# Kernel tuning notes

Measured on AMD Instinct MI355X. Metric: run time of the kernel, lower is better.

## Reference

```python
import jax, jax.numpy as jnp
import numpy as np

N_NODES = 50000
N_EDGES = 640000
HID = 128
EDGE_FEAT = 4
NUM_G = 20
R_MIN, R_MAX = 0.0, 10.0

def setup_inputs() -> dict:
    key = jax.random.key(0)
    ks = jax.random.split(key, 16)
    s = lambda d: 1.0 / np.sqrt(d)
    return {
        'h': jax.random.normal(ks[0], (N_NODES, HID), jnp.float32),
        'x': jax.random.normal(ks[1], (N_NODES, 3), jnp.float32),
        'edge_index': jax.random.randint(ks[2], (2, N_EDGES), 0, N_NODES, dtype=jnp.int64),
        'mask_ligand': jnp.ones((N_NODES,), jnp.float32),
        'edge_attr': jax.random.normal(ks[3], (N_EDGES, EDGE_FEAT), jnp.float32),
        'We1': jax.random.normal(ks[4], (2*HID+EDGE_FEAT+NUM_G, HID), jnp.float32) * s(2*HID+EDGE_FEAT+NUM_G),
        'be1': jnp.zeros((HID,), jnp.float32),
        'We2': jax.random.normal(ks[5], (HID, HID), jnp.float32) * s(HID),
        'be2': jnp.zeros((HID,), jnp.float32),
        'Winf': jax.random.normal(ks[6], (HID, 1), jnp.float32) * s(HID),
        'binf': jnp.zeros((1,), jnp.float32),
        'Wx1': jax.random.normal(ks[7], (HID, HID), jnp.float32) * s(HID),
        'bx1': jnp.zeros((HID,), jnp.float32),
        'Wx2': jax.random.normal(ks[8], (HID, 1), jnp.float32) * 0.001 * s(HID),
        'Wn1': jax.random.normal(ks[9], (2*HID, HID), jnp.float32) * s(2*HID),
        'bn1': jnp.zeros((HID,), jnp.float32),
        'Wn2': jax.random.normal(ks[10], (HID, HID), jnp.float32) * s(HID),
        'bn2': jnp.zeros((HID,), jnp.float32),
    }

def reference(h, x, edge_index, mask_ligand, edge_attr,
              We1, be1, We2, be2, Winf, binf, Wx1, bx1, Wx2, Wn1, bn1, Wn2, bn2):
    n = h.shape[0]
    src, dst = edge_index[0], edge_index[1]
    hi, hj = h[dst], h[src]                      # [E, H] gathers
    rel_x = x[dst] - x[src]                      # [E, 3]
    d_sq = jnp.sum(rel_x**2, axis=-1, keepdims=True)  # [E, 1]
    d = jnp.sqrt(d_sq + 1e-8)
    # GaussianSmearing(r_min=0, r_max=10, num_gaussians=20)
    offset = jnp.linspace(R_MIN, R_MAX, NUM_G, dtype=h.dtype)
    coeff = -0.5 / (offset[1] - offset[0])**2
    d_feat = jnp.exp(coeff * (d - offset)**2)    # [E, 20]
    edge_feat = jnp.concatenate([d_feat, edge_attr], axis=-1)
    # edge MLP (2 layers, silu, act_last=True)
    z = jnp.concatenate([hi, hj, edge_feat], axis=-1)
    mij = jax.nn.silu(jax.nn.silu(z @ We1 + be1) @ We2 + be2)  # [E, H]
    eij = jax.nn.sigmoid(mij @ Winf + binf)      # [E, 1]
    mi = jax.ops.segment_sum(mij * eij, dst, num_segments=n)   # [N, H]
    # node MLP (2 layers, silu, no act on last)
    nz = jnp.concatenate([mi, h], axis=-1)
    h_out = h + (jax.nn.silu(nz @ Wn1 + bn1) @ Wn2 + bn2)
    # coordinate update
    xg = jnp.tanh(jax.nn.silu(mij @ Wx1 + bx1) @ Wx2)          # [E, 1]
    delta_x = jax.ops.segment_sum(rel_x / (d + 1.0) * xg, dst, num_segments=n)
    x_out = x + delta_x * mask_ligand[:, None]
    return h_out, x_out
```

## Files before the change

### kernel.cpp

```cpp
#include <hip/hip_runtime.h>
#include <math.h>

#define NN 50000
#define NE 640000
#define H 128
#define EPB 64
#define NPB 64
#define ZB 296
#define BB 136
#define KP1 288
#define NZB 264
#define NBPAD 50176
#define HISTB (NE / 256)
#define CONVB 464
#define ALLOCB (NBPAD / 256)
#define HCONVB 3125
#define N4OUT ((NN * H + NN * 3) / 4)
#define ZOB ((N4OUT + 255) / 256)

typedef __attribute__((ext_vector_type(8))) unsigned short u16x8;
typedef __attribute__((ext_vector_type(8))) __bf16 bf16x8;
typedef __attribute__((ext_vector_type(2))) __bf16 bf16x2;
typedef __attribute__((ext_vector_type(4))) float f32x4;

__device__ __forceinline__ float frcp(float x) {
#if __has_builtin(__builtin_amdgcn_rcpf)
    return __builtin_amdgcn_rcpf(x);
#else
    return 1.0f / x;
#endif
}

__device__ __forceinline__ float silu_f(float v) {
    return v * frcp(1.0f + __expf(-v));
}

__device__ __forceinline__ float sigmoid_f(float v) {
    return frcp(1.0f + __expf(-v));
}

__device__ __forceinline__ float tanh_f(float v) {
    return 1.0f - 2.0f * frcp(1.0f + __expf(2.0f * v));
}

__device__ __forceinline__ unsigned short f2bf(float f) {
    unsigned int u = __builtin_bit_cast(unsigned int, f);
    u += 0x7FFFu + ((u >> 16) & 1u);
    return (unsigned short)(u >> 16);
}

__device__ __forceinline__ float bf2f(unsigned short s) {
    unsigned int u = ((unsigned int)s) << 16;
    return __builtin_bit_cast(float, u);
}

__device__ __forceinline__ unsigned int pkbf(float lo, float hi) {
#if __has_builtin(__builtin_amdgcn_cvt_pk_bf16_f32)
    bf16x2 v = __builtin_amdgcn_cvt_pk_bf16_f32(lo, hi);
    unsigned int r; __builtin_memcpy(&r, &v, 4); return r;
#else
    return (unsigned int)f2bf(lo) | ((unsigned int)f2bf(hi) << 16);
#endif
}

__device__ __forceinline__ f32x4 mfma16(u16x8 a, u16x8 b, f32x4 c) {
    return __builtin_amdgcn_mfma_f32_16x16x32_bf16(
        __builtin_bit_cast(bf16x8, a), __builtin_bit_cast(bf16x8, b), c, 0, 0, 0);
}

__global__ __launch_bounds__(256) void init_small_kernel(
    float4* __restrict__ p, int n4)
{
    int i = blockIdx.x * 256 + threadIdx.x;
    if (i < n4) p[i] = make_float4(0.f, 0.f, 0.f, 0.f);
}

__global__ __launch_bounds__(256) void hist_conv_zero_hconv_kernel(
    const int* __restrict__ ei, int* __restrict__ cnt, int histBlocks,
    const float* __restrict__ We1, const float* __restrict__ We2,
    const float* __restrict__ Wx1, const float* __restrict__ Wn1,
    const float* __restrict__ Wn2,
    unsigned short* __restrict__ w1t, unsigned short* __restrict__ w2t,
    unsigned short* __restrict__ wx1t, unsigned short* __restrict__ wn1t,
    unsigned short* __restrict__ wn2t,
    float4* __restrict__ out4,
    const float* __restrict__ h, unsigned short* __restrict__ hb)
{
    int b = blockIdx.x, t = threadIdx.x;
    if (b < histBlocks) {
        atomicAdd(&cnt[ei[NE + b * 256 + t]], 1);
        return;
    }
    b -= histBlocks;
    if (b < CONVB) {
        int i = b * 256 + t;
        const int S1 = 128 * KP1;
        const int S2 = 128 * 128;
        const int S3 = 128 * 256;
        if (i < S1) {
            int n = i / KP1, k = i % KP1;
            w1t[i] = (k < 280) ? f2bf(We1[k * H + n]) : (unsigned short)0;
        } else if (i < S1 + S2) {
            int j = i - S1; int n = j / H, k = j % H;
            w2t[j] = f2bf(We2[k * H + n]);
        } else if (i < S1 + 2 * S2) {
            int j = i - S1 - S2; int n = j / H, k = j % H;
            wx1t[j] = f2bf(Wx1[k * H + n]);
        } else if (i < S1 + 2 * S2 + S3) {
            int j = i - S1 - 2 * S2; int n = j / 256, k = j % 256;
            wn1t[j] = f2bf(Wn1[k * H + n]);
        } else if (i < S1 + 3 * S2 + S3) {
            int j = i - S1 - 2 * S2 - S3; int n = j / H, k = j % H;
            wn2t[j] = f2bf(Wn2[k * H + n]);
        }
        return;
    }
    b -= CONVB;
    if (b < ZOB) {
        int i = b * 256 + t;
        if (i < N4OUT) out4[i] = make_float4(0.f, 0.f, 0.f, 0.f);
        return;
    }
    b -= ZOB;
    int j = b * 256 + t;
    const float4* hp = (const float4*)h + (size_t)j * 2;
    float4 a = hp[0], c = hp[1];
    uint4 pk = { pkbf(a.x, a.y), pkbf(a.z, a.w), pkbf(c.x, c.y), pkbf(c.z, c.w) };
    ((uint4*)hb)[j] = pk;
}

__global__ __launch_bounds__(256) void alloc_kernel(
    const int* __restrict__ cnt, int* __restrict__ cur, int* __restrict__ gtot)
{
    int t = threadIdx.x;
    int d = blockIdx.x * 256 + t;
    int v = cnt[d];
    int incl = v;
    #pragma unroll
    for (int o = 1; o < 64; o <<= 1) {
        int u = __shfl_up(incl, o, 64);
        if ((t & 63) >= o) incl += u;
    }
    int total = __shfl(incl, 63, 64);
    int base = 0;
    if ((t & 63) == 63) base = atomicAdd(gtot, total);
    base = __shfl(base, 63, 64);
    cur[d] = base + incl - v;
}

__global__ __launch_bounds__(256) void scatter_kernel(
    const int* __restrict__ ei, const float* __restrict__ edge_attr,
    int* __restrict__ cur, uint4* __restrict__ epay)
{
    int i = blockIdx.x * 256 + threadIdx.x;
    int s = ei[i], d = ei[NE + i];
    float4 ea = ((const float4*)edge_attr)[i];
    int p = atomicAdd(&cur[d], 1);
    uint4 pv = { (unsigned)s, (unsigned)d, pkbf(ea.x, ea.y), pkbf(ea.z, ea.w) };
    epay[p] = pv;
}

__global__ __launch_bounds__(512, 6) void edge_kernel(
    const float* __restrict__ h, const float* __restrict__ x,
    const int* __restrict__ ei, const float* __restrict__ edge_attr,
    const unsigned short* __restrict__ w1t, const float* __restrict__ be1,
    const unsigned short* __restrict__ w2t, const float* __restrict__ be2,
    const float* __restrict__ Winf, const float* __restrict__ binf,
    const unsigned short* __restrict__ wx1t, const float* __restrict__ bx1,
    const float* __restrict__ Wx2,
    const uint4* __restrict__ epay, const unsigned short* __restrict__ hb,
    float* __restrict__ mi, float* __restrict__ dx)
{
    __shared__ unsigned short zs[EPB * ZB];
    __shared__ float relx_s[EPB][3];
    __shared__ float eij_s[EPB];
    __shared__ float xg_s[EPB];
    __shared__ float epart[8][EPB];
    __shared__ float xpart[8][EPB];
    __shared__ int dst_s[EPB];
    __shared__ float winf_s[H];
    __shared__ float wx2_s[H];

    unsigned short* m1 = zs;
    unsigned short* m2 = zs + EPB * BB;

    const int t = threadIdx.x;
    const int e0 = blockIdx.x * EPB;
    const bool srt = (epay != nullptr);

    if (t >= 128 && t < 256) {
        winf_s[t - 128] = Winf[t - 128];
        wx2_s[t - 128] = Wx2[t - 128];
    }

    {
        int e = t >> 3, l = t & 7;
        unsigned short* zr = zs + e * ZB;
        if (srt) {
            uint4 pv = epay[e0 + e];
            const uint4* hd = (const uint4*)(hb + (size_t)pv.y * H);
            const uint4* hs = (const uint4*)(hb + (size_t)pv.x * H);
            uint4 a0 = hd[l * 2], a1 = hd[l * 2 + 1];
            *(uint4*)(zr + l * 16) = a0;
            *(uint4*)(zr + l * 16 + 8) = a1;
            uint4 c0 = hs[l * 2], c1 = hs[l * 2 + 1];
            *(uint4*)(zr + 128 + l * 16) = c0;
            *(uint4*)(zr + 128 + l * 16 + 8) = c1;
        } else {
            int s = ei[e0 + e], d = ei[NE + e0 + e];
            const float4* hd = (const float4*)(h + (size_t)d * H);
            const float4* hs = (const float4*)(h + (size_t)s * H);
            float4 v0 = hd[l * 4 + 0], v1 = hd[l * 4 + 1];
            float4 v2 = hd[l * 4 + 2], v3 = hd[l * 4 + 3];
            uint4 p0 = { pkbf(v0.x, v0.y), pkbf(v0.z, v0.w), pkbf(v1.x, v1.y), pkbf(v1.z, v1.w) };
            uint4 p1 = { pkbf(v2.x, v2.y), pkbf(v2.z, v2.w), pkbf(v3.x, v3.y), pkbf(v3.z, v3.w) };
            *(uint4*)(zr + l * 16) = p0;
            *(uint4*)(zr + l * 16 + 8) = p1;
            float4 w0 = hs[l * 4 + 0], w1 = hs[l * 4 + 1];
            float4 w2 = hs[l * 4 + 2], w3 = hs[l * 4 + 3];
            uint4 q0 = { pkbf(w0.x, w0.y), pkbf(w0.z, w0.w), pkbf(w1.x, w1.y), pkbf(w1.z, w1.w) };
            uint4 q1 = { pkbf(w2.x, w2.y), pkbf(w2.z, w2.w), pkbf(w3.x, w3.y), pkbf(w3.z, w3.w) };
            *(uint4*)(zr + 128 + l * 16) = q0;
            *(uint4*)(zr + 128 + l * 16 + 8) = q1;
        }
    }
    if (t < EPB) {
        unsigned short* zr = zs + t * ZB;
        int s, d;
        if (srt) {
            uint4 pv = epay[e0 + t];
            s = (int)pv.x; d = (int)pv.y;
            *(unsigned int*)(zr + 276) = pv.z;
            *(unsigned int*)(zr + 278) = pv.w;
        } else {
            s = ei[e0 + t]; d = ei[NE + e0 + t];
            #pragma unroll
            for (int j = 0; j < 4; j++)
                zr[276 + j] = f2bf(edge_attr[(size_t)(e0 + t) * 4 + j]);
        }
        dst_s[t] = d;
        float rx = x[d * 3 + 0] - x[s * 3 + 0];
        float ry = x[d * 3 + 1] - x[s * 3 + 1];
        float rz = x[d * 3 + 2] - x[s * 3 + 2];
        float d2 = rx * rx + ry * ry + rz * rz;
        float dd = sqrtf(d2 + 1e-8f);
        float inv = frcp(dd + 1.0f);
        relx_s[t][0] = rx * inv;
        relx_s[t][1] = ry * inv;
        relx_s[t][2] = rz * inv;
        const float step = 10.0f / 19.0f;
        const float coeff = -0.5f / (step * step);
        #pragma unroll
        for (int g = 0; g < 20; g++) {
            float df = dd - step * (float)g;
            zr[256 + g] = f2bf(__expf(coeff * df * df));
        }
        #pragma unroll
        for (int j = 280; j < ZB; j++) zr[j] = 0;
    }
    __syncthreads();

    const int wv = t >> 6, lane = t & 63;
    const int quad = lane >> 4, r16 = lane & 15;
    const int F = wv * 16;
    const int f0 = F + quad * 4;

    {
        f32x4 acc[4] = {};
        #pragma unroll
        for (int ks = 0; ks < KP1 / 32; ks++) {
            int ko = ks * 32 + quad * 8;
            u16x8 a = *(const u16x8*)(w1t + (size_t)(F + r16) * KP1 + ko);
            #pragma unroll
            for (int ci = 0; ci < 4; ci++) {
                u16x8 b = *(const u16x8*)(zs + (ci * 16 + r16) * ZB + ko);
                acc[ci] = mfma16(a, b, acc[ci]);
            }
        }
        __syncthreads();
        float4 bv = *(const float4*)(be1 + f0);
        #pragma unroll
        for (int ci = 0; ci < 4; ci++) {
            int e = ci * 16 + r16;
            float s0 = silu_f(acc[ci][0] + bv.x);
            float s1 = silu_f(acc[ci][1] + bv.y);
            float s2 = silu_f(acc[ci][2] + bv.z);
            float s3 = silu_f(acc[ci][3] + bv.w);
            uint2 p = { pkbf(s0, s1), pkbf(s2, s3) };
            *(uint2*)(m1 + e * BB + f0) = p;
        }
    }
    __syncthreads();

    {
        f32x4 acc[4] = {};
        #pragma unroll
        for (int ks = 0; ks < H / 32; ks++) {
            int ko = ks * 32 + quad * 8;
            u16x8 a = *(const u16x8*)(w2t + (size_t)(F + r16) * H + ko);
            #pragma unroll
            for (int ci = 0; ci < 4; ci++) {
                u16x8 b = *(const u16x8*)(m1 + (ci * 16 + r16) * BB + ko);
                acc[ci] = mfma16(a, b, acc[ci]);
            }
        }
        float4 bv = *(const float4*)(be2 + f0);
        float4 wf = *(const float4*)(winf_s + f0);
        float ep[4];
        #pragma unroll
        for (int ci = 0; ci < 4; ci++) {
            int e = ci * 16 + r16;
            float s0 = silu_f(acc[ci][0] + bv.x);
            float s1 = silu_f(acc[ci][1] + bv.y);
            float s2 = silu_f(acc[ci][2] + bv.z);
            float s3 = silu_f(acc[ci][3] + bv.w);
            ep[ci] = s0 * wf.x + s1 * wf.y + s2 * wf.z + s3 * wf.w;
            uint2 p = { pkbf(s0, s1), pkbf(s2, s3) };
            *(uint2*)(m2 + e * BB + f0) = p;
        }
        #pragma unroll
        for (int ci = 0; ci < 4; ci++) {
            ep[ci] += __shfl_xor(ep[ci], 16, 64);
            ep[ci] += __shfl_xor(ep[ci], 32, 64);
        }
        if (quad == 0) {
            #pragma unroll
            for (int ci = 0; ci < 4; ci++)
                epart[wv][ci * 16 + r16] = ep[ci];
        }
    }
    __syncthreads();

    if (t < EPB) {
        float s = binf[0];
        #pragma unroll
        for (int w = 0; w < 8; w++) s += epart[w][t];
        eij_s[t] = sigmoid_f(s);
    }

    {
        f32x4 acc[4] = {};
        #pragma unroll
        for (int ks = 0; ks < H / 32; ks++) {
            int ko = ks * 32 + quad * 8;
            u16x8 a = *(const u16x8*)(wx1t + (size_t)(F + r16) * H + ko);
            #pragma unroll
            for (int ci = 0; ci < 4; ci++) {
                u16x8 b = *(const u16x8*)(m2 + (ci * 16 + r16) * BB + ko);
                acc[ci] = mfma16(a, b, acc[ci]);
            }
        }
        float4 bv = *(const float4*)(bx1 + f0);
        float4 wf = *(const float4*)(wx2_s + f0);
        float xp[4];
        #pragma unroll
        for (int ci = 0; ci < 4; ci++) {
            xp[ci] = silu_f(acc[ci][0] + bv.x) * wf.x
                   + silu_f(acc[ci][1] + bv.y) * wf.y
                   + silu_f(acc[ci][2] + bv.z) * wf.z
                   + silu_f(acc[ci][3] + bv.w) * wf.w;
        }
        #pragma unroll
        for (int ci = 0; ci < 4; ci++) {
            xp[ci] += __shfl_xor(xp[ci], 16, 64);
            xp[ci] += __shfl_xor(xp[ci], 32, 64);
        }
        if (quad == 0) {
            #pragma unroll
            for (int ci = 0; ci < 4; ci++)
                xpart[wv][ci * 16 + r16] = xp[ci];
        }
    }
    __syncthreads();

    if (t < EPB) {
        float xs = 0.f;
        #pragma unroll
        for (int w = 0; w < 8; w++) xs += xpart[w][t];
        xg_s[t] = tanh_f(xs);
    }
    __syncthreads();

    if (t < 128) {
        const int k = t;
        float acc = 0.f;
        int rs = 0;
        #pragma unroll
        for (int c = 0; c < EPB; c += 8) {
            float v[8];
            #pragma unroll
            for (int j = 0; j < 8; j++)
                v[j] = bf2f(m2[(c + j) * BB + k]) * eij_s[c + j];
            #pragma unroll
            for (int j = 0; j < 8; j++) {
                int e = c + j;
                acc += v[j];
                if (e == EPB - 1 || dst_s[e + 1] != dst_s[e]) {
                    float* p = &mi[(size_t)dst_s[e] * H + k];
                    if (srt && rs > 0 && e < EPB - 1) *p = acc;
                    else atomicAdd(p, acc);
                    acc = 0.f;
                    rs = e + 1;
                }
            }
        }
    } else if (t < 131) {
        const int dd = t - 128;
        float acc = 0.f;
        int rs = 0;
        #pragma unroll
        for (int c = 0; c < EPB; c += 8) {
            float v[8];
            #pragma unroll
            for (int j = 0; j < 8; j++)
                v[j] = relx_s[c + j][dd] * xg_s[c + j];
            #pragma unroll
            for (int j = 0; j < 8; j++) {
                int e = c + j;
                acc += v[j];
                if (e == EPB - 1 || dst_s[e + 1] != dst_s[e]) {
                    float* p = &dx[(size_t)dst_s[e] * 3 + dd];
                    if (srt && rs > 0 && e < EPB - 1) *p = acc;
                    else atomicAdd(p, acc);
                    acc = 0.f;
                    rs = e + 1;
                }
            }
        }
    }
}

__global__ __launch_bounds__(512, 6) void node_kernel(
    const float* __restrict__ h, const float* __restrict__ x,
    const float* __restrict__ mask,
    const unsigned short* __restrict__ wn1t, const float* __restrict__ bn1,
    const unsigned short* __restrict__ wn2t, const float* __restrict__ bn2,
    const unsigned short* __restrict__ hb,
    float* __restrict__ mi_hout, float* __restrict__ dx_xout)
{
    __shared__ unsigned short nzs[NPB * NZB];

    unsigned short* nbuf = nzs;

    const int t = threadIdx.x;
    const int n0 = blockIdx.x * NPB;

    {
        int r = t >> 3, l = t & 7;
        int n = n0 + r;
        unsigned short* zr = nzs + r * NZB;
        if (n < NN) {
            const float4* mi4 = (const float4*)(mi_hout + (size_t)n * H);
            float4 v0 = mi4[l * 4 + 0], v1 = mi4[l * 4 + 1];
            float4 v2 = mi4[l * 4 + 2], v3 = mi4[l * 4 + 3];
            uint4 p0 = { pkbf(v0.x, v0.y), pkbf(v0.z, v0.w), pkbf(v1.x, v1.y), pkbf(v1.z, v1.w) };
            uint4 p1 = { pkbf(v2.x, v2.y), pkbf(v2.z, v2.w), pkbf(v3.x, v3.y), pkbf(v3.z, v3.w) };
            *(uint4*)(zr + l * 16) = p0;
            *(uint4*)(zr + l * 16 + 8) = p1;
            if (hb) {
                const uint4* hs = (const uint4*)(hb + (size_t)n * H);
                *(uint4*)(zr + 128 + l * 16) = hs[l * 2];
                *(uint4*)(zr + 128 + l * 16 + 8) = hs[l * 2 + 1];
            } else {
                const float4* h4 = (const float4*)(h + (size_t)n * H);
                float4 w0 = h4[l * 4 + 0], w1 = h4[l * 4 + 1];
                float4 w2 = h4[l * 4 + 2], w3 = h4[l * 4 + 3];
                uint4 q0 = { pkbf(w0.x, w0.y), pkbf(w0.z, w0.w), pkbf(w1.x, w1.y), pkbf(w1.z, w1.w) };
                uint4 q1 = { pkbf(w2.x, w2.y), pkbf(w2.z, w2.w), pkbf(w3.x, w3.y), pkbf(w3.z, w3.w) };
                *(uint4*)(zr + 128 + l * 16) = q0;
                *(uint4*)(zr + 128 + l * 16 + 8) = q1;
            }
        } else {
            uint4 zf = {0u, 0u, 0u, 0u};
            *(uint4*)(zr + l * 16) = zf;
            *(uint4*)(zr + l * 16 + 8) = zf;
            *(uint4*)(zr + 128 + l * 16) = zf;
            *(uint4*)(zr + 128 + l * 16 + 8) = zf;
        }
    }

    float xo = 0.f;
    int xn = -1, xdim = 0;
    if (t < NPB * 3) {
        int r = t / 3; xdim = t % 3;
        int n = n0 + r;
        if (n < NN) {
            xn = n;
            xo = x[(size_t)n * 3 + xdim] + dx_xout[(size_t)n * 3 + xdim] * mask[n];
        }
    }
    __syncthreads();

    if (xn >= 0) dx_xout[(size_t)xn * 3 + xdim] = xo;

    const int wv = t >> 6, lane = t & 63;
    const int quad = lane >> 4, r16 = lane & 15;
    const int F = wv * 16;
    const int f0 = F + quad * 4;

    {
        f32x4 acc[4] = {};
        #pragma unroll
        for (int ks = 0; ks < 2 * H / 32; ks++) {
            int ko = ks * 32 + quad * 8;
            u16x8 a = *(const u16x8*)(wn1t + (size_t)(F + r16) * (2 * H) + ko);
            #pragma unroll
            for (int ci = 0; ci < 4; ci++) {
                u16x8 b = *(const u16x8*)(nzs + (ci * 16 + r16) * NZB + ko);
                acc[ci] = mfma16(a, b, acc[ci]);
            }
        }
        __syncthreads();
        float4 bv = *(const float4*)(bn1 + f0);
        #pragma unroll
        for (int ci = 0; ci < 4; ci++) {
            int e = ci * 16 + r16;
            float s0 = silu_f(acc[ci][0] + bv.x);
            float s1 = silu_f(acc[ci][1] + bv.y);
            float s2 = silu_f(acc[ci][2] + bv.z);
            float s3 = silu_f(acc[ci][3] + bv.w);
            uint2 p = { pkbf(s0, s1), pkbf(s2, s3) };
            *(uint2*)(nbuf + e * BB + f0) = p;
        }
    }
    __syncthreads();

    {
        f32x4 acc[4] = {};
        #pragma unroll
        for (int ks = 0; ks < H / 32; ks++) {
            int ko = ks * 32 + quad * 8;
            u16x8 a = *(const u16x8*)(wn2t + (size_t)(F + r16) * H + ko);
            #pragma unroll
            for (int ci = 0; ci < 4; ci++) {
                u16x8 b = *(const u16x8*)(nbuf + (ci * 16 + r16) * BB + ko);
                acc[ci] = mfma16(a, b, acc[ci]);
            }
        }
        float4 bv = *(const float4*)(bn2 + f0);
        #pragma unroll
        for (int ci = 0; ci < 4; ci++) {
            int n = n0 + ci * 16 + r16;
            if (n < NN) {
                float4 hv = *(const float4*)(h + (size_t)n * H + f0);
                float4 o;
                o.x = hv.x + acc[ci][0] + bv.x;
                o.y = hv.y + acc[ci][1] + bv.y;
                o.z = hv.z + acc[ci][2] + bv.z;
                o.w = hv.w + acc[ci][3] + bv.w;
                *(float4*)(mi_hout + (size_t)n * H + f0) = o;
            }
        }
    }
}

extern "C" void kernel_launch(void* const* d_in, const int* in_sizes, int n_in,
                              void* d_out, int out_size, void* d_ws, size_t ws_size,
                              hipStream_t stream) {
    const float* h     = (const float*)d_in[0];
    const float* x     = (const float*)d_in[1];
    const int*   ei    = (const int*)d_in[2];
    const float* mask  = (const float*)d_in[3];
    const float* eattr = (const float*)d_in[4];
    const float* We1   = (const float*)d_in[5];
    const float* be1   = (const float*)d_in[6];
    const float* We2   = (const float*)d_in[7];
    const float* be2   = (const float*)d_in[8];
    const float* Winf  = (const float*)d_in[9];
    const float* binf  = (const float*)d_in[10];
    const float* Wx1   = (const float*)d_in[11];
    const float* bx1   = (const float*)d_in[12];
    const float* Wx2   = (const float*)d_in[13];
    const float* Wn1   = (const float*)d_in[14];
    const float* bn1   = (const float*)d_in[15];
    const float* Wn2   = (const float*)d_in[16];
    const float* bn2   = (const float*)d_in[17];

    float* mi = (float*)d_out;
    float* dx = mi + (size_t)NN * H;

    char* wsb  = (char*)d_ws;
    unsigned short* w1t  = (unsigned short*)wsb;
    unsigned short* w2t  = w1t + 128 * KP1;
    unsigned short* wx1t = w2t + 128 * H;
    unsigned short* wn1t = wx1t + 128 * H;
    unsigned short* wn2t = wn1t + 128 * 256;

    const size_t OFF_CNT  = 262144;
    const size_t OFF_GTOT = OFF_CNT + (size_t)NBPAD * 4;
    const size_t OFF_CUR  = OFF_GTOT + 16;
    const size_t OFF_HB   = OFF_CUR + (size_t)NBPAD * 4;
    const size_t OFF_EPAY = OFF_HB + (size_t)NN * H * 2;
    const size_t WS_NEED  = OFF_EPAY + (size_t)NE * 16;

    int*   cnt  = (int*)(wsb + OFF_CNT);
    int*   gtot = (int*)(wsb + OFF_GTOT);
    int*   cur  = (int*)(wsb + OFF_CUR);
    unsigned short* hb = (unsigned short*)(wsb + OFF_HB);
    uint4* epay = (uint4*)(wsb + OFF_EPAY);

    const bool full = (ws_size >= WS_NEED);

    if (full) {
        const int n4c = (int)((OFF_CUR - OFF_CNT) / 16);
        init_small_kernel<<<(n4c + 255) / 256, 256, 0, stream>>>(
            (float4*)(wsb + OFF_CNT), n4c);
    }

    {
        int hb_ = full ? HISTB : 0;
        int hc_ = full ? HCONVB : 0;
        hist_conv_zero_hconv_kernel<<<hb_ + CONVB + ZOB + hc_, 256, 0, stream>>>(
            ei, cnt, hb_, We1, We2, Wx1, Wn1, Wn2,
            w1t, w2t, wx1t, wn1t, wn2t, (float4*)d_out, h, hb);
    }

    if (full) {
        alloc_kernel<<<ALLOCB, 256, 0, stream>>>(cnt, cur, gtot);
        scatter_kernel<<<NE / 256, 256, 0, stream>>>(ei, eattr, cur, epay);
    }

    edge_kernel<<<NE / EPB, 512, 0, stream>>>(
        h, x, ei, eattr, w1t, be1, w2t, be2, Winf, binf, wx1t, bx1, Wx2,
        full ? epay : (const uint4*)nullptr,
        full ? hb : (const unsigned short*)nullptr,
        mi, dx);

    node_kernel<<<(NN + NPB - 1) / NPB, 512, 0, stream>>>(
        h, x, mask, wn1t, bn1, wn2t, bn2,
        full ? hb : (const unsigned short*)nullptr,
        mi, dx);
}
```

Baseline: 424.8 us.

## Parallelize edge-block segmented reduction across all threads with shuffle-based carry

The per-block segment sum over 64 edges was done serially by 128 threads, one per feature column, and 3 threads for coordinates. It is now split so each of 512 threads handles a 16-edge slice of one column. Partial segments that cross slices are combined with a segmented scan built from wave shuffles, and only the leading segment's value takes the carried-in sum. The intent is to shorten the serial tail after the edge MLP, at the cost of extra shuffles and possibly more atomics at slice boundaries.

```diff
diff --git a/kernel.cpp b/kernel.cpp
--- a/kernel.cpp
+++ b/kernel.cpp
@@ -381,51 +381,84 @@
     }
     __syncthreads();
 
-    if (t < 128) {
-        const int k = t;
-        float acc = 0.f;
-        int rs = 0;
-        #pragma unroll
-        for (int c = 0; c < EPB; c += 8) {
+    {
+        const int k  = wv * 16 + r16;
+        const int gs = quad * 16;
+        float acc = 0.f, lead = 0.f;
+        int lead_e = 0;
+        bool open = true;
+        #pragma unroll
+        for (int c = 0; c < 16; c += 8) {
             float v[8];
             #pragma unroll
             for (int j = 0; j < 8; j++)
-                v[j] = bf2f(m2[(c + j) * BB + k]) * eij_s[c + j];
+                v[j] = bf2f(m2[(gs + c + j) * BB + k]) * eij_s[gs + c + j];
             #pragma unroll
             for (int j = 0; j < 8; j++) {
-                int e = c + j;
+                int e = gs + c + j;
                 acc += v[j];
-                if (e == EPB - 1 || dst_s[e + 1] != dst_s[e]) {
-                    float* p = &mi[(size_t)dst_s[e] * H + k];
-                    if (srt && rs > 0 && e < EPB - 1) *p = acc;
+                bool tb = (e < EPB - 1) && (dst_s[e + 1] != dst_s[e]);
+                if (tb || e == EPB - 1) {
+                    if (open) { lead = acc; lead_e = e; open = false; }
+                    else {
+                        float* p = &mi[(size_t)dst_s[e] * H + k];
+                        if (srt && e < EPB - 1) *p = acc;
+                        else atomicAdd(p, acc);
+                    }
+                    acc = 0.f;
+                }
+            }
+        }
+        float xv = acc; int fb = open ? 0 : 1;
+        float xi = __shfl_up(xv, 16, 64); int fi = __shfl_up(fb, 16, 64);
+        if (quad >= 1 && !fb) { xv += xi; fb = fi; }
+        xi = __shfl_up(xv, 32, 64); fi = __shfl_up(fb, 32, 64);
+        if (quad >= 2 && !fb) { xv += xi; fb = fi; }
+        float cin = __shfl_up(xv, 16, 64);
+        int fprev = __shfl_up(fb, 16, 64);
+        bool sb = (quad == 0) ? true : (fprev == 0);
+        if (quad == 0) cin = 0.f;
+        if (!open) {
+            float val = lead + cin;
+            float* p = &mi[(size_t)dst_s[lead_e] * H + k];
+            if (srt && !sb && lead_e < EPB - 1) *p = val;
+            else atomicAdd(p, val);
+        }
+    }
+    if (t < 12) {
+        const int dd = t % 3, q2 = t / 3, gs = q2 * 16;
+        float acc = 0.f, lead = 0.f;
+        int lead_e = 0;
+        bool open = true;
+        #pragma unroll
+        for (int j = 0; j < 16; j++) {
+            int e = gs + j;
+            acc += relx_s[e][dd] * xg_s[e];
+            bool tb = (e < EPB - 1) && (dst_s[e + 1] != dst_s[e]);
+            if (tb || e == EPB - 1) {
+                if (open) { lead = acc; lead_e = e; open = false; }
+                else {
+                    float* p = &dx[(size_t)dst_s[e] * 3 + dd];
+                    if (srt && e < EPB - 1) *p = acc;
                     else atomicAdd(p, acc);
-                    acc = 0.f;
-                    rs = e + 1;
                 }
-            }
-        }
-    } else if (t < 131) {
-        const int dd = t - 128;
-        float acc = 0.f;
-        int rs = 0;
-        #pragma unroll
-        for (int c = 0; c < EPB; c += 8) {
-            float v[8];
-            #pragma unroll
-            for (int j = 0; j < 8; j++)
-                v[j] = relx_s[c + j][dd] * xg_s[c + j];
-            #pragma unroll
-            for (int j = 0; j < 8; j++) {
-                int e = c + j;
-                acc += v[j];
-                if (e == EPB - 1 || dst_s[e + 1] != dst_s[e]) {
-                    float* p = &dx[(size_t)dst_s[e] * 3 + dd];
-                    if (srt && rs > 0 && e < EPB - 1) *p = acc;
-                    else atomicAdd(p, acc);
-                    acc = 0.f;
-                    rs = e + 1;
-                }
-            }
+                acc = 0.f;
+            }
+        }
+        float xv = acc; int fb = open ? 0 : 1;
+        float xi = __shfl_up(xv, 3, 64); int fi = __shfl_up(fb, 3, 64);
+        if (q2 >= 1 && !fb) { xv += xi; fb = fi; }
+        xi = __shfl_up(xv, 6, 64); fi = __shfl_up(fb, 6, 64);
+        if (q2 >= 2 && !fb) { xv += xi; fb = fi; }
+        float cin = __shfl_up(xv, 3, 64);
+        int fprev = __shfl_up(fb, 3, 64);
+        bool sb = (q2 == 0) ? true : (fprev == 0);
+        if (q2 == 0) cin = 0.f;
+        if (!open) {
+            float val = lead + cin;
+            float* p = &dx[(size_t)dst_s[lead_e] * 3 + dd];
+            if (srt && !sb && lead_e < EPB - 1) *p = val;
+            else atomicAdd(p, val);
         }
     }
 }
```

Result: no change. 425.8 us (+0.2%).
